# Performance work log

Measured on AMD Instinct MI355X. Metric: run time of the kernel, lower is better.

The kernel has to match this reference:

```python
import jax, jax.numpy as jnp
import numpy as np

B, C, T, V = 64, 64, 128, 25   # batch, in_channels, frames, joints
R = 8                          # rel_channels = in_channels // rel_reduction
TS = 9                         # time_step (temporal taps of dynamic adjacency)
OUT = 64                       # out_channels (conv3)


def setup_inputs() -> dict:
    key = jax.random.key(0)
    ks = jax.random.split(key, 10)
    p = lambda k, shape: jax.random.normal(k, shape, jnp.float32) * 0.05
    return {
        'x':  jax.random.normal(ks[0], (B, C, T, V), jnp.float32),
        'A':  jax.random.normal(ks[1], (V, V), jnp.float32) * 0.1,
        'W1': p(ks[2], (R, C)),       'b1': p(ks[3], (R,)),
        'W2': p(ks[4], (R, C)),       'b2': p(ks[5], (R,)),
        'W4': p(ks[6], (C * TS, R)),  'b4': p(ks[7], (C * TS,)),
        'W3': p(ks[8], (OUT, C)),     'b3': p(ks[9], (OUT,)),
    }


def reference(x, A, W1, b1, W2, b2, W4, b4, W3, b3):
    alpha = 1.0
    # conv1/conv2: 1x1 Conv2d then mean over time (dim -2). 1x1 conv is linear,
    # so mean(conv(x)) == einsum/T + bias.  -> (B, R, V)
    x1 = jnp.einsum('rc,bctv->brv', W1, x) / T + b1[None, :, None]
    x2 = jnp.einsum('rc,bctv->brv', W2, x) / T + b2[None, :, None]
    # tanh relation: (B, R, V, 1) - (B, R, 1, V) -> (B, R, V, V)
    rel = jnp.tanh(x1[:, :, :, None] - x2[:, :, None, :])
    # conv4 (1x1): rel_channels -> C*TS dynamic adjacency, + static A
    Adyn = jnp.einsum('or,brij->boij', W4, rel) + b4[None, :, None, None]
    Adyn = Adyn * alpha + A[None, None]                      # (B, C*TS, V, V)
    # reshape(B, C, TS, V, V).permute(0,1,3,4,2): per-(b,c) temporal graph kernel
    Wk = Adyn.reshape(B, C, TS, V, V).transpose(0, 1, 3, 4, 2)  # (B, C, V, V, TS)
    # x -> (B, C, V, T), causal left-pad by TS-1 (matches F.pad(x, (TS-1, 0)))
    xp = jnp.pad(x.transpose(0, 1, 3, 2), ((0, 0), (0, 0), (0, 0), (TS - 1, 0)))
    # Grouped conv1d loop over V vertices, fused into TS tap-wise einsums:
    # z[b,c,t,i] = sum_{v,k} xp[b,c,v,t+k] * Wk[b,c,v,i,k]   (stride=1)
    z = jnp.zeros((B, C, T, V), x.dtype)
    for k in range(TS):  # small fixed tap loop
        z = z + jnp.einsum('bcvt,bcvi->bcti', xp[..., k:k + T], Wk[..., k])
    # conv3: 1x1 Conv2d C -> OUT
    out = jnp.einsum('oc,bctv->botv', W3, z) + b3[None, :, None, None]
    return out
```

## Files before the change

### kernel.cpp

```cpp
#include <hip/hip_runtime.h>
#include <hip/hip_bf16.h>

#define BB 64
#define CC 64
#define TT_ 128
#define VV 25
#define RR 8
#define TS_ 9
#define OO 64
#define VCH 5

typedef __hip_bfloat16 bf16;
typedef __attribute__((ext_vector_type(8))) short short8;
typedef __attribute__((ext_vector_type(4))) short s16x4;
typedef __attribute__((ext_vector_type(4))) float f32x4;

__device__ __forceinline__ unsigned short f2b(float f) {
    bf16 h = __float2bfloat16(f);
    return __builtin_bit_cast(unsigned short, h);
}

__global__ __launch_bounds__(256) void k_mean(const float* __restrict__ x,
                                              float* __restrict__ xm) {
    __shared__ float smf[800];
    int bc = blockIdx.x;
    int tid = threadIdx.x;
    const float4* p4 = (const float4*)(x + (size_t)bc * TT_ * VV);
    if (tid < 200) {
        float4 a = p4[tid];
        float4 b = p4[tid + 200];
        float4 c = p4[tid + 400];
        float4 d = p4[tid + 600];
        float4 s;
        s.x = a.x + b.x + c.x + d.x;
        s.y = a.y + b.y + c.y + d.y;
        s.z = a.z + b.z + c.z + d.z;
        s.w = a.w + b.w + c.w + d.w;
        ((float4*)smf)[tid] = s;
    }
    __syncthreads();
    if (tid < VV) {
        float tot = 0.f;
        #pragma unroll
        for (int m = 0; m < 32; m++) tot += smf[tid + VV * m];
        xm[bc * VV + tid] = tot * (1.0f / TT_);
    }
}

__global__ __launch_bounds__(256) void k_rel(const float* __restrict__ xm,
                                             const float* __restrict__ W1,
                                             const float* __restrict__ b1,
                                             const float* __restrict__ W2,
                                             const float* __restrict__ b2,
                                             float* __restrict__ rel) {
    __shared__ float xms[CC * VV];
    __shared__ float x1s[RR][VCH];
    __shared__ float x2s[RR][VV];
    int b = blockIdx.x / 5, g = blockIdx.x % 5;
    int v0 = g * VCH;
    int tid = threadIdx.x;
    for (int i = tid; i < CC * VV; i += 256) xms[i] = xm[b * CC * VV + i];
    __syncthreads();
    if (tid < 240) {
        if (tid < 40) {
            int r = tid / VCH, vl = tid % VCH;
            float s1 = b1[r];
            for (int c = 0; c < CC; c++) s1 += W1[r * CC + c] * xms[c * VV + v0 + vl];
            x1s[r][vl] = s1;
        } else {
            int t = tid - 40;
            int r = t / VV, i = t % VV;
            float s2 = b2[r];
            for (int c = 0; c < CC; c++) s2 += W2[r * CC + c] * xms[c * VV + i];
            x2s[r][i] = s2;
        }
    }
    __syncthreads();
    float* relb = rel + (size_t)b * VV * VV * RR + (size_t)v0 * VV * RR;
    for (int idx = tid; idx < VCH * VV * RR; idx += 256) {
        int r = idx % RR;
        int i = (idx / RR) % VV;
        int vl = idx / (RR * VV);
        float d = x1s[r][vl] - x2s[r][i];
        float e = __expf(2.0f * d);
        relb[idx] = (e - 1.0f) / (e + 1.0f);
    }
}

__global__ __launch_bounds__(256) void k_z(const float* __restrict__ x,
                                           const float* __restrict__ Ag,
                                           const float* __restrict__ W4,
                                           const float* __restrict__ b4,
                                           const float* __restrict__ rel,
                                           bf16* __restrict__ zws) {
    __shared__ __align__(16) unsigned short xpadB[136 * 40];
    __shared__ __align__(16) unsigned short AdbS[TS_ * 32 * 40];

    int tid = threadIdx.x;
    int bc = blockIdx.x;
    int b = bc / CC, c = bc % CC;

    if (tid < 128) ((unsigned int*)xpadB)[(tid >> 4) * 20 + (tid & 15)] = 0u;
    for (int id = tid; id < 128 * 7; id += 256) {
        int r = 8 + id / 7, v = 25 + id % 7;
        xpadB[r * 40 + v] = 0;
    }
    for (int id = tid; id < TS_ * 25 * 7; id += 256) {
        int s = id / 175, rem = id % 175;
        int i = rem / 7, v = 25 + rem % 7;
        AdbS[(s * 32 + i) * 40 + v] = 0;
    }
    const float4* xg4 = (const float4*)(x + (size_t)bc * TT_ * VV);
    for (int i4 = tid; i4 < TT_ * VV / 4; i4 += 256) {
        float4 f = xg4[i4];
        int idx = i4 * 4;
        int t = idx / VV, v = idx - t * VV;
        float fe[4] = {f.x, f.y, f.z, f.w};
        #pragma unroll
        for (int e = 0; e < 4; e++) {
            xpadB[(t + 8) * 40 + v] = f2b(fe[e]);
            v++;
            if (v == VV) { v = 0; t++; }
        }
    }

    const float* relb = rel + (size_t)b * VV * VV * RR;
    const float* W4c = W4 + c * TS_ * RR;
    const float* b4c = b4 + c * TS_;
    for (int task = tid; task < VV * VV; task += 256) {
        int v = task / VV, i = task % VV;
        const float4* r4 = (const float4*)(relb + (size_t)task * RR);
        float4 ra = r4[0], rb_ = r4[1];
        float av = Ag[task];
        #pragma unroll
        for (int s = 0; s < TS_; s++) {
            float a2 = b4c[s] + av;
            a2 += W4c[s*8+0] * ra.x  + W4c[s*8+1] * ra.y
                + W4c[s*8+2] * ra.z  + W4c[s*8+3] * ra.w;
            a2 += W4c[s*8+4] * rb_.x + W4c[s*8+5] * rb_.y
                + W4c[s*8+6] * rb_.z + W4c[s*8+7] * rb_.w;
            AdbS[(s * 32 + i) * 40 + v] = f2b(a2);
        }
    }
    __syncthreads();

    int lane = tid & 63, wv = tid >> 6;
    int ml = lane & 15, qd = lane >> 4;
    f32x4 acc00 = {0.f, 0.f, 0.f, 0.f};
    f32x4 acc01 = acc00, acc10 = acc00, acc11 = acc00;
    int rowA0 = (wv * 2) * 16 + ml;
    #pragma unroll
    for (int s = 0; s < TS_; s++) {
        short8 a0 = *(const short8*)&xpadB[(rowA0 + s) * 40 + qd * 8];
        short8 a1 = *(const short8*)&xpadB[(rowA0 + 16 + s) * 40 + qd * 8];
        short8 b0 = *(const short8*)&AdbS[(s * 32 + ml) * 40 + qd * 8];
        short8 b1 = *(const short8*)&AdbS[(s * 32 + 16 + ml) * 40 + qd * 8];
        acc00 = __builtin_amdgcn_mfma_f32_16x16x32_bf16(a0, b0, acc00, 0, 0, 0);
        acc01 = __builtin_amdgcn_mfma_f32_16x16x32_bf16(a0, b1, acc01, 0, 0, 0);
        acc10 = __builtin_amdgcn_mfma_f32_16x16x32_bf16(a1, b0, acc10, 0, 0, 0);
        acc11 = __builtin_amdgcn_mfma_f32_16x16x32_bf16(a1, b1, acc11, 0, 0, 0);
    }

    bf16* zb = zws + (size_t)bc * TT_ * VV;
    int t0 = (wv * 2) * 16 + qd * 4;
    int i0 = ml, i1 = 16 + ml;
    #pragma unroll
    for (int r = 0; r < 4; r++) {
        zb[(t0 + r) * VV + i0]      = __float2bfloat16(acc00[r]);
        zb[(t0 + 16 + r) * VV + i0] = __float2bfloat16(acc10[r]);
    }
    if (i1 < VV) {
        #pragma unroll
        for (int r = 0; r < 4; r++) {
            zb[(t0 + r) * VV + i1]      = __float2bfloat16(acc01[r]);
            zb[(t0 + 16 + r) * VV + i1] = __float2bfloat16(acc11[r]);
        }
    }
}

__global__ __launch_bounds__(256) void k_conv3(const bf16* __restrict__ zws,
                                               const float* __restrict__ W3,
                                               const float* __restrict__ b3,
                                               float* __restrict__ out) {
    __shared__ __align__(16) unsigned short w3b[OO * 72];
    __shared__ __align__(16) unsigned short zl[CC * 130];
    __shared__ float b3l[OO];
    int tid = threadIdx.x;
    int b = blockIdx.x / 25, tile = blockIdx.x % 25;
    int tj0 = tile * 128;

    if (tid < OO) b3l[tid] = b3[tid];
    const float4* W3v = (const float4*)W3;
    for (int idx = tid; idx < OO * CC / 4; idx += 256) {
        float4 f = W3v[idx];
        int o = idx >> 4, c4 = (idx & 15) * 4;
        s16x4 s4;
        s4[0] = (short)f2b(f.x);
        s4[1] = (short)f2b(f.y);
        s4[2] = (short)f2b(f.z);
        s4[3] = (short)f2b(f.w);
        *(s16x4*)&w3b[o * 72 + c4] = s4;
    }
    const unsigned int* zg = (const unsigned int*)(zws + (size_t)b * CC * (TT_ * VV));
    for (int idu = tid; idu < CC * 64; idu += 256) {
        int c = idu >> 6, ju = idu & 63;
        ((unsigned int*)zl)[c * 65 + ju] = zg[c * 1600 + (tj0 >> 1) + ju];
    }
    __syncthreads();

    int lane = tid & 63, wv = tid >> 6;
    int ml = lane & 15, qd = lane >> 4;
    f32x4 acc[4][2];
    #pragma unroll
    for (int m = 0; m < 4; m++)
        #pragma unroll
        for (int nl = 0; nl < 2; nl++) acc[m][nl] = (f32x4){0.f, 0.f, 0.f, 0.f};

    #pragma unroll
    for (int k0 = 0; k0 < 2; k0++) {
        short8 a[4];
        #pragma unroll
        for (int m = 0; m < 4; m++)
            a[m] = *(const short8*)&w3b[(m * 16 + ml) * 72 + k0 * 32 + qd * 8];
        #pragma unroll
        for (int nl = 0; nl < 2; nl++) {
            int col = (2 * wv + nl) * 16 + ml;
            int cb = k0 * 32 + qd * 8;
            short8 bf;
            #pragma unroll
            for (int j = 0; j < 8; j++)
                bf[j] = (short)zl[(cb + j) * 130 + col];
            #pragma unroll
            for (int m = 0; m < 4; m++)
                acc[m][nl] = __builtin_amdgcn_mfma_f32_16x16x32_bf16(a[m], bf, acc[m][nl], 0, 0, 0);
        }
    }

    float* ob = out + (size_t)b * OO * (TT_ * VV) + tj0;
    #pragma unroll
    for (int m = 0; m < 4; m++)
        #pragma unroll
        for (int nl = 0; nl < 2; nl++) {
            int col = (2 * wv + nl) * 16 + ml;
            #pragma unroll
            for (int r = 0; r < 4; r++) {
                int o = m * 16 + qd * 4 + r;
                ob[(size_t)o * (TT_ * VV) + col] = acc[m][nl][r] + b3l[o];
            }
        }
}

extern "C" void kernel_launch(void* const* d_in, const int* in_sizes, int n_in,
                              void* d_out, int out_size, void* d_ws, size_t ws_size,
                              hipStream_t stream) {
    const float* x  = (const float*)d_in[0];
    const float* A  = (const float*)d_in[1];
    const float* W1 = (const float*)d_in[2];
    const float* b1 = (const float*)d_in[3];
    const float* W2 = (const float*)d_in[4];
    const float* b2 = (const float*)d_in[5];
    const float* W4 = (const float*)d_in[6];
    const float* b4 = (const float*)d_in[7];
    const float* W3 = (const float*)d_in[8];
    const float* b3 = (const float*)d_in[9];
    float* out = (float*)d_out;

    char* ws = (char*)d_ws;
    float* xm   = (float*)(ws);
    float* rel  = (float*)(ws + 409600);
    bf16*  zws  = (bf16*)(ws + 1689600);

    k_mean <<<BB * CC, 256, 0, stream>>>(x, xm);
    k_rel  <<<BB * 5,  256, 0, stream>>>(xm, W1, b1, W2, b2, rel);
    k_z    <<<BB * CC, 256, 0, stream>>>(x, A, W4, b4, rel, zws);
    k_conv3<<<BB * 25, 256, 0, stream>>>(zws, W3, b3, out);
}
```

Measured before the change: 161.2 us.

## Compute dynamic adjacency via MFMA with bias/A folded into augmented K

```diff
diff --git a/kernel.cpp b/kernel.cpp
--- a/kernel.cpp
+++ b/kernel.cpp
@@ -93,59 +93,108 @@
                                            const float* __restrict__ b4,
                                            const float* __restrict__ rel,
                                            bf16* __restrict__ zws) {
-    __shared__ __align__(16) unsigned short xpadB[136 * 40];
+    __shared__ __align__(16) unsigned short ushare[136 * 40];
     __shared__ __align__(16) unsigned short AdbS[TS_ * 32 * 40];
+    unsigned short* relbf = ushare;
+    unsigned short* w4f2  = ushare + 5120;
+    unsigned short* xpadB = ushare;
 
     int tid = threadIdx.x;
     int bc = blockIdx.x;
     int b = bc / CC, c = bc % CC;
+    int lane = tid & 63, wv = tid >> 6;
+    int ml = lane & 15, qd = lane >> 4;
+
+    for (int id = tid; id < TS_ * 25 * 7; id += 256) {
+        int s = id / 175, rem = id % 175;
+        int i = rem / 7, v = 25 + rem % 7;
+        AdbS[(s * 32 + i) * 40 + v] = 0;
+    }
+    {
+        int s = tid >> 4, k = tid & 15;
+        if (tid < 256) {
+            float val = 0.f;
+            if (s < TS_) {
+                if (k < 8)       val = W4[(c * TS_ + s) * RR + k];
+                else if (k == 8) val = b4[c * TS_ + s];
+                else if (k == 9) val = 1.0f;
+            }
+            w4f2[tid] = f2b(val);
+        }
+    }
+    {
+        const float4* r4g = (const float4*)(rel + (size_t)b * VV * VV * RR);
+        for (int i4 = tid; i4 < 1250; i4 += 256) {
+            float4 f = r4g[i4];
+            s16x4 s4;
+            s4[0] = (short)f2b(f.x); s4[1] = (short)f2b(f.y);
+            s4[2] = (short)f2b(f.z); s4[3] = (short)f2b(f.w);
+            *(s16x4*)&relbf[i4 * 4] = s4;
+        }
+    }
+    const float4* xg4 = (const float4*)(x + (size_t)bc * TT_ * VV);
+    float4 xr0 = xg4[tid];
+    float4 xr1 = xg4[tid + 256];
+    float4 xr2 = xg4[tid + 512];
+    float4 xr3 = {0.f, 0.f, 0.f, 0.f};
+    if (tid < 32) xr3 = xg4[tid + 768];
+    __syncthreads();
+
+    {
+        short8 afrag = {0, 0, 0, 0, 0, 0, 0, 0};
+        if (qd < 2) afrag = *(const short8*)&w4f2[ml * 16 + qd * 8];
+        #pragma unroll
+        for (int rep = 0; rep < 10; rep++) {
+            int tile = wv + rep * 4;
+            int task = tile * 16 + ml;
+            short8 bfrag = {0, 0, 0, 0, 0, 0, 0, 0};
+            if (qd == 0) {
+                bfrag = *(const short8*)&relbf[task * 8];
+            } else if (qd == 1) {
+                int ti = task < 625 ? task : 624;
+                bfrag[0] = (short)0x3F80;
+                bfrag[1] = (short)f2b(Ag[ti]);
+            }
+            f32x4 acc = {0.f, 0.f, 0.f, 0.f};
+            acc = __builtin_amdgcn_mfma_f32_16x16x32_bf16(afrag, bfrag, acc, 0, 0, 0);
+            if (task < 625) {
+                int v = task / 25;
+                int ii = task - v * 25;
+                if (qd < 2) {
+                    #pragma unroll
+                    for (int r = 0; r < 4; r++)
+                        AdbS[((qd * 4 + r) * 32 + ii) * 40 + v] = f2b(acc[r]);
+                } else if (qd == 2) {
+                    AdbS[(8 * 32 + ii) * 40 + v] = f2b(acc[0]);
+                }
+            }
+        }
+    }
+    __syncthreads();
 
     if (tid < 128) ((unsigned int*)xpadB)[(tid >> 4) * 20 + (tid & 15)] = 0u;
     for (int id = tid; id < 128 * 7; id += 256) {
         int r = 8 + id / 7, v = 25 + id % 7;
         xpadB[r * 40 + v] = 0;
     }
-    for (int id = tid; id < TS_ * 25 * 7; id += 256) {
-        int s = id / 175, rem = id % 175;
-        int i = rem / 7, v = 25 + rem % 7;
-        AdbS[(s * 32 + i) * 40 + v] = 0;
-    }
-    const float4* xg4 = (const float4*)(x + (size_t)bc * TT_ * VV);
-    for (int i4 = tid; i4 < TT_ * VV / 4; i4 += 256) {
-        float4 f = xg4[i4];
-        int idx = i4 * 4;
-        int t = idx / VV, v = idx - t * VV;
-        float fe[4] = {f.x, f.y, f.z, f.w};
-        #pragma unroll
-        for (int e = 0; e < 4; e++) {
-            xpadB[(t + 8) * 40 + v] = f2b(fe[e]);
-            v++;
-            if (v == VV) { v = 0; t++; }
-        }
-    }
-
-    const float* relb = rel + (size_t)b * VV * VV * RR;
-    const float* W4c = W4 + c * TS_ * RR;
-    const float* b4c = b4 + c * TS_;
-    for (int task = tid; task < VV * VV; task += 256) {
-        int v = task / VV, i = task % VV;
-        const float4* r4 = (const float4*)(relb + (size_t)task * RR);
-        float4 ra = r4[0], rb_ = r4[1];
-        float av = Ag[task];
-        #pragma unroll
-        for (int s = 0; s < TS_; s++) {
-            float a2 = b4c[s] + av;
-            a2 += W4c[s*8+0] * ra.x  + W4c[s*8+1] * ra.y
-                + W4c[s*8+2] * ra.z  + W4c[s*8+3] * ra.w;
-            a2 += W4c[s*8+4] * rb_.x + W4c[s*8+5] * rb_.y
-                + W4c[s*8+6] * rb_.z + W4c[s*8+7] * rb_.w;
-            AdbS[(s * 32 + i) * 40 + v] = f2b(a2);
-        }
-    }
-    __syncthreads();
-
-    int lane = tid & 63, wv = tid >> 6;
-    int ml = lane & 15, qd = lane >> 4;
+    {
+        auto put4 = [&](int i4, float4 f) {
+            int idx = i4 * 4;
+            int t = idx / VV, v = idx - t * VV;
+            float fe[4] = {f.x, f.y, f.z, f.w};
+            #pragma unroll
+            for (int e = 0; e < 4; e++) {
+                xpadB[(t + 8) * 40 + v] = f2b(fe[e]);
+                if (++v == VV) { v = 0; t++; }
+            }
+        };
+        put4(tid, xr0);
+        put4(tid + 256, xr1);
+        put4(tid + 512, xr2);
+        if (tid < 32) put4(tid + 768, xr3);
+    }
+    __syncthreads();
+
     f32x4 acc00 = {0.f, 0.f, 0.f, 0.f};
     f32x4 acc01 = acc00, acc10 = acc00, acc11 = acc00;
     int rowA0 = (wv * 2) * 16 + ml;
```

After: 184.1 us. +14.2%, slower.
